# Optimization experiments

Hardware: AMD Instinct MI355X
Metric: run time of the kernel (lower is better)

## Reference

```python
import jax, jax.numpy as jnp
import numpy as np

VOCAB = 32000
DIM = 1024
HID = 4096
MAXLEN = 2048
NH = 2       # number of sequential LowRankLinearAttention layers
KD = 64      # key_dim hardcoded in the module
B = 2
L = 2048


def setup_inputs() -> dict:
    key = jax.random.key(0)
    ks = jax.random.split(key, 12)
    def rn(k, shape, scale):
        return jax.random.normal(k, shape, dtype=jnp.float32) * scale
    return {
        "input_indices": jax.random.randint(ks[0], (B, L), 0, VOCAB),
        "token_embed": rn(ks[1], (VOCAB, DIM), 0.02),
        "pos_embed": rn(ks[2], (MAXLEN, DIM), 0.02),
        # per-layer attention projections (stored [in, out]; x @ W == torch Linear)
        "Wq": rn(ks[3], (NH, DIM, KD), DIM ** -0.5),
        "Wk": rn(ks[4], (NH, DIM, KD), DIM ** -0.5),
        "Wv": rn(ks[5], (NH, DIM, KD), DIM ** -0.5),
        "Wo": rn(ks[6], (NH, KD, DIM), KD ** -0.5),
        "norm_g": jnp.ones((NH, DIM), jnp.float32),
        "norm_b": jnp.zeros((NH, DIM), jnp.float32),
        "out_norm_g": jnp.ones((DIM,), jnp.float32),
        "out_norm_b": jnp.zeros((DIM,), jnp.float32),
        "W1": rn(ks[7], (DIM, HID), DIM ** -0.5),
        "b1": jnp.zeros((HID,), jnp.float32),
        "W2": rn(ks[8], (HID, VOCAB), HID ** -0.5),
        "b2": jnp.zeros((VOCAB,), jnp.float32),
    }


def _layernorm(x, g, b, eps=1e-5):
    m = jnp.mean(x, axis=-1, keepdims=True)
    v = jnp.var(x, axis=-1, keepdims=True)
    return (x - m) / jnp.sqrt(v + eps) * g + b


def _lowrank_linear_attn(x, Wq, Wk, Wv, Wo):
    # x: [B,L,D]; Q,K,V: [B,L,k]
    Q = jax.nn.elu(x @ Wq) + 1.0
    K = jax.nn.elu(x @ Wk) + 1.0
    V = x @ Wv
    # causal prefix sums of outer products K_t V_t^T -> [B,L,k,k]
    KV_sum = jnp.cumsum(K[..., :, None] * V[..., None, :], axis=1)
    K_sum = jnp.cumsum(K, axis=1)
    num = jnp.einsum('blk,blkj->blj', Q, KV_sum)          # [B,L,k]
    den = jnp.einsum('blk,blk->bl', Q, K_sum)[..., None]  # [B,L,1]
    return (num / (den + 1e-6)) @ Wo


def reference(input_indices, token_embed, pos_embed, Wq, Wk, Wv, Wo,
              norm_g, norm_b, out_norm_g, out_norm_b, W1, b1, W2, b2):
    seq_len = input_indices.shape[1]
    x = token_embed[input_indices] + pos_embed[jnp.arange(seq_len)]
    for i in range(Wq.shape[0]):
        x = x + _lowrank_linear_attn(x, Wq[i], Wk[i], Wv[i], Wo[i])
        x = _layernorm(x, norm_g[i], norm_b[i])
    x = _layernorm(x, out_norm_g, out_norm_b)
    h = jax.nn.gelu(x @ W1 + b1, approximate=False)  # torch nn.GELU default = erf
    logits = h @ W2 + b2
    return logits
```

## Files before the change

kernel.cpp:

```cpp
#include <hip/hip_runtime.h>

typedef __attribute__((ext_vector_type(4))) float  f4;
typedef __attribute__((ext_vector_type(2))) float  f2;
typedef __attribute__((ext_vector_type(4))) unsigned short us4;
typedef __attribute__((ext_vector_type(8))) short  s8;
typedef __attribute__((ext_vector_type(4))) float  f32x4;

__device__ __forceinline__ unsigned short f2bf(float f) {
  unsigned u = __float_as_uint(f);
  u += 0x7fffu + ((u >> 16) & 1u);
  return (unsigned short)(u >> 16);
}
__device__ __forceinline__ float elu1(float x) { return x > 0.f ? x + 1.f : __expf(x); }
__device__ __forceinline__ float gelu_erf(float x) { return 0.5f * x * (1.f + erff(x * 0.70710678118654752f)); }

__device__ __forceinline__ void async16(const void* g, void* l) {
  __builtin_amdgcn_global_load_lds((const __attribute__((address_space(1))) void*)g,
                                   (__attribute__((address_space(3))) void*)l, 16, 0, 0);
}

__device__ __forceinline__ void rawbar() {
  asm volatile("s_barrier" ::: "memory");
}

__device__ __forceinline__ unsigned l2u(const void* p) {
  return (unsigned)(size_t)(const __attribute__((address_space(3))) char*)p;
}
template<int OFF>
__device__ __forceinline__ void dsr(s8& d, unsigned base) {
  asm volatile("ds_read_b128 %0, %1 offset:%2" : "=v"(d) : "v"(base), "i"(OFF));
}

__global__ __launch_bounds__(256) void embed_kernel(
    const int* __restrict__ idx, const float* __restrict__ tok,
    const float* __restrict__ pos, float* __restrict__ X, unsigned short* __restrict__ XB)
{
  int g = blockIdx.x * 256 + threadIdx.x;
  int t = g >> 8;
  int c4 = (g & 255) * 4;
  int l = t & 2047;
  int tk = idx[t];
  f4 v = *(const f4*)(tok + (size_t)tk * 1024 + c4);
  f4 p = *(const f4*)(pos + (size_t)l * 1024 + c4);
  v += p;
  *(f4*)(X + (size_t)t * 1024 + c4) = v;
  us4 o = { f2bf(v[0]), f2bf(v[1]), f2bf(v[2]), f2bf(v[3]) };
  *(us4*)(XB + (size_t)t * 1024 + c4) = o;
}

__global__ __launch_bounds__(256) void transpose_cvt(
    const float* __restrict__ src, unsigned short* __restrict__ dst, int N, int K)
{
  __shared__ unsigned short t[64][72];
  int k0 = blockIdx.x * 64, n0 = blockIdx.y * 64;
  int tid = threadIdx.x;
#pragma unroll
  for (int i = 0; i < 4; ++i) {
    int f = tid + i * 256;
    int r = f >> 4, c4 = (f & 15) * 4;
    f4 v = *(const f4*)(src + (size_t)(k0 + r) * N + n0 + c4);
    us4 o = { f2bf(v[0]), f2bf(v[1]), f2bf(v[2]), f2bf(v[3]) };
    *(us4*)&t[r][c4] = o;
  }
  __syncthreads();
#pragma unroll
  for (int i = 0; i < 4; ++i) {
    int f = tid + i * 256;
    int nr = f >> 4, kc4 = (f & 15) * 4;
    us4 o = { t[kc4 + 0][nr], t[kc4 + 1][nr], t[kc4 + 2][nr], t[kc4 + 3][nr] };
    *(us4*)(dst + (size_t)(n0 + nr) * K + k0 + kc4) = o;
  }
}

template<int EPI, int BF32>
__global__ __launch_bounds__(256) void gemm_bt(
    const unsigned short* __restrict__ A, const unsigned short* __restrict__ Bt,
    const float* __restrict__ Bf, const float* __restrict__ bias,
    void* __restrict__ Cv, int M, int N, int K, int mtiles)
{
  __shared__ unsigned short As[128 * 32];
  __shared__ unsigned short Bs[128 * 32];
  int bid = blockIdx.x;
  int mt = bid % mtiles, nt = bid / mtiles;
  int m0 = mt * 128, n0 = nt * 128;
  int tid = threadIdx.x, lane = tid & 63, w = tid >> 6;
  int wm = (w & 1) * 64, wn = (w >> 1) * 64;

  int c0 = w * 128 + lane, c1 = c0 + 64;
  size_t aO0 = (size_t)(m0 + (c0 >> 2)) * K + (size_t)((c0 & 3) * 8);
  size_t aO1 = (size_t)(m0 + (c1 >> 2)) * K + (size_t)((c1 & 3) * 8);
  size_t bO0 = (size_t)(n0 + (c0 >> 2)) * K + (size_t)((c0 & 3) * 8);
  size_t bO1 = (size_t)(n0 + (c1 >> 2)) * K + (size_t)((c1 & 3) * 8);
  unsigned short* lA0 = As + (w * 128) * 8;
  unsigned short* lA1 = As + (w * 128 + 64) * 8;
  unsigned short* lB0 = Bs + (w * 128) * 8;
  unsigned short* lB1 = Bs + (w * 128 + 64) * 8;

  f32x4 acc[4][4];
  f32x4 zz = {0.f, 0.f, 0.f, 0.f};
#pragma unroll
  for (int i = 0; i < 4; ++i)
#pragma unroll
    for (int j = 0; j < 4; ++j) acc[i][j] = zz;

  int rr = lane & 15, kh = (lane >> 4) * 8;
  const unsigned short* Ar = As + (wm + rr) * 32 + kh;
  const unsigned short* Br = Bs + (wn + rr) * 32 + kh;

  for (int k0 = 0; k0 < K; k0 += 32) {
    async16(A + aO0 + k0, lA0);
    async16(A + aO1 + k0, lA1);
    if constexpr (!BF32) {
      async16(Bt + bO0 + k0, lB0);
      async16(Bt + bO1 + k0, lB1);
    } else {
#pragma unroll
      for (int i = 0; i < 4; ++i) {
        int f = tid + i * 256;
        int kr = f >> 5, c4 = (f & 31) * 4;
        f4 v = *(const f4*)(Bf + (size_t)(k0 + kr) * N + n0 + c4);
#pragma unroll
        for (int e = 0; e < 4; ++e) Bs[(c4 + e) * 32 + kr] = f2bf(v[e]);
      }
    }
    __syncthreads();
    s8 af[4], bfr[4];
#pragma unroll
    for (int mi = 0; mi < 4; ++mi) af[mi] = *(const s8*)(Ar + mi * 512);
#pragma unroll
    for (int ni = 0; ni < 4; ++ni) bfr[ni] = *(const s8*)(Br + ni * 512);
#pragma unroll
    for (int mi = 0; mi < 4; ++mi)
#pragma unroll
      for (int ni = 0; ni < 4; ++ni)
        acc[mi][ni] = __builtin_amdgcn_mfma_f32_16x16x32_bf16(af[mi], bfr[ni], acc[mi][ni], 0, 0, 0);
    __syncthreads();
  }

  int cr = (lane >> 4) * 4;
#pragma unroll
  for (int mi = 0; mi < 4; ++mi) {
#pragma unroll
    for (int ni = 0; ni < 4; ++ni) {
      int gc = n0 + wn + ni * 16 + rr;
      float bv = (EPI > 0) ? bias[gc] : 0.f;
#pragma unroll
      for (int r = 0; r < 4; ++r) {
        int gr = m0 + wm + mi * 16 + cr + r;
        float v = acc[mi][ni][r] + bv;
        if constexpr (EPI == 1) {
          ((unsigned short*)Cv)[(size_t)gr * N + gc] = f2bf(gelu_erf(v));
        } else {
          ((float*)Cv)[(size_t)gr * N + gc] = v;
        }
      }
    }
  }
}

template<int EPI>
__global__ __launch_bounds__(512) void gemm2(
    const unsigned short* __restrict__ A, const unsigned short* __restrict__ Bt,
    const float* __restrict__ bias, void* __restrict__ Cv,
    int M, int N, int K, int mtiles)
{
  __shared__ __align__(16) char A0r[32768];
  __shared__ __align__(16) char B0r[32768];
  __shared__ __align__(16) char A1r[32768];
  __shared__ __align__(16) char B1r[32768];

  const int tid = threadIdx.x, lane = tid & 63, w = tid >> 6;
  const int wm = w >> 2, wn = w & 3;
  const int NT = K >> 6;

  int nwg = gridDim.x, orig = blockIdx.x;
  int q = nwg >> 3, r = nwg & 7;
  int xcd = orig & 7, lin = orig >> 3;
  int swz = (xcd < r ? xcd * (q + 1) : r * (q + 1) + (xcd - r) * q) + lin;
  int mt = swz % mtiles, nt = swz / mtiles;
  int m0 = mt * 256, n0 = nt * 256;

  const size_t klane8 = (size_t)((lane >> 4) << 3);
  const size_t arow0 = (size_t)(m0 + w * 32 + (lane & 15)) * K;
  const size_t arow1 = arow0 + (size_t)16 * K;
  const size_t brow0 = (size_t)(n0 + w * 32 + (lane & 15)) * K;
  const size_t brow1 = brow0 + (size_t)16 * K;

  auto stgA = [&](char* reg, int kt, int kb) {
    int ktc = kt < NT ? kt : NT - 1;
    size_t kk = (size_t)ktc * 64 + (size_t)(kb * 32) + klane8;
    char* d = reg + w * 4096 + kb * 1024;
    async16(A + arow0 + kk, d);
    async16(A + arow1 + kk, d + 2048);
  };
  auto stgB = [&](char* reg, int kt, int kb) {
    int ktc = kt < NT ? kt : NT - 1;
    size_t kk = (size_t)ktc * 64 + (size_t)(kb * 32) + klane8;
    char* d = reg + w * 4096 + kb * 1024;
    async16(Bt + brow0 + kk, d);
    async16(Bt + brow1 + kk, d + 2048);
  };

  const unsigned AB0 = l2u(A0r + wm * 16384 + lane * 16);
  const unsigned BB0 = l2u(B0r + wn * 8192 + lane * 16);
  const unsigned AB1 = l2u(A1r + wm * 16384 + lane * 16);
  const unsigned BB1 = l2u(B1r + wn * 8192 + lane * 16);

  f32x4 acc[8][4];
  f32x4 zz = {0.f, 0.f, 0.f, 0.f};
#pragma unroll
  for (int i = 0; i < 8; ++i)
#pragma unroll
    for (int j = 0; j < 4; ++j) acc[i][j] = zz;

  stgA(A0r, 0, 0); stgA(A0r, 0, 1); stgB(B0r, 0, 0); stgB(B0r, 0, 1);
  stgA(A1r, 1, 0); stgA(A1r, 1, 1); stgB(B1r, 1, 0); stgB(B1r, 1, 1);
  asm volatile("s_waitcnt vmcnt(8)" ::: "memory");
  rawbar();

  for (int t = 0; t < NT; ++t) {
    const int odd = t & 1;
    const unsigned AB = odd ? AB1 : AB0;
    const unsigned BB = odd ? BB1 : BB0;
    char* Ad = odd ? A1r : A0r;
    char* Bd = odd ? B1r : B0r;

    s8 bf[8], af[16];
    dsr<(0 * 2 + 0) * 1024>(bf[0], BB);
    dsr<(0 * 2 + 1) * 1024>(bf[1], BB);
    dsr<(1 * 2 + 0) * 1024>(bf[2], BB);
    dsr<(1 * 2 + 1) * 1024>(bf[3], BB);
    dsr<(2 * 2 + 0) * 1024>(bf[4], BB);
    dsr<(2 * 2 + 1) * 1024>(bf[5], BB);
    dsr<(3 * 2 + 0) * 1024>(bf[6], BB);
    dsr<(3 * 2 + 1) * 1024>(bf[7], BB);
    dsr<(0 * 2 + 0) * 1024>(af[0], AB);
    dsr<(0 * 2 + 1) * 1024>(af[1], AB);
    dsr<(1 * 2 + 0) * 1024>(af[2], AB);
    dsr<(1 * 2 + 1) * 1024>(af[3], AB);
    dsr<(2 * 2 + 0) * 1024>(af[4], AB);
    dsr<(2 * 2 + 1) * 1024>(af[5], AB);
    dsr<(3 * 2 + 0) * 1024>(af[6], AB);
    dsr<(3 * 2 + 1) * 1024>(af[7], AB);
    dsr<(4 * 2 + 0) * 1024>(af[8], AB);
    dsr<(4 * 2 + 1) * 1024>(af[9], AB);
    dsr<(5 * 2 + 0) * 1024>(af[10], AB);
    dsr<(5 * 2 + 1) * 1024>(af[11], AB);
    dsr<(6 * 2 + 0) * 1024>(af[12], AB);
    dsr<(6 * 2 + 1) * 1024>(af[13], AB);
    dsr<(7 * 2 + 0) * 1024>(af[14], AB);
    dsr<(7 * 2 + 1) * 1024>(af[15], AB);

    asm volatile("s_waitcnt lgkmcnt(12)" ::: "memory");
    __builtin_amdgcn_sched_barrier(0);
    __builtin_amdgcn_s_setprio(1);
#pragma unroll
    for (int ni = 0; ni < 4; ++ni) {
#pragma unroll
      for (int f = 0; f < 2; ++f) {
        acc[f][ni] = __builtin_amdgcn_mfma_f32_16x16x32_bf16(af[f * 2 + 0], bf[ni * 2 + 0], acc[f][ni], 0, 0, 0);
        acc[f][ni] = __builtin_amdgcn_mfma_f32_16x16x32_bf16(af[f * 2 + 1], bf[ni * 2 + 1], acc[f][ni], 0, 0, 0);
      }
    }
    __builtin_amdgcn_s_setprio(0);
    asm volatile("s_waitcnt lgkmcnt(8)" ::: "memory");
    __builtin_amdgcn_sched_barrier(0);
    __builtin_amdgcn_s_setprio(1);
#pragma unroll
    for (int ni = 0; ni < 4; ++ni) {
#pragma unroll
      for (int f = 2; f < 4; ++f) {
        acc[f][ni] = __builtin_amdgcn_mfma_f32_16x16x32_bf16(af[f * 2 + 0], bf[ni * 2 + 0], acc[f][ni], 0, 0, 0);
        acc[f][ni] = __builtin_amdgcn_mfma_f32_16x16x32_bf16(af[f * 2 + 1], bf[ni * 2 + 1], acc[f][ni], 0, 0, 0);
      }
    }
    __builtin_amdgcn_s_setprio(0);
    asm volatile("s_waitcnt lgkmcnt(4)" ::: "memory");
    __builtin_amdgcn_sched_barrier(0);
    __builtin_amdgcn_s_setprio(1);
#pragma unroll
    for (int ni = 0; ni < 4; ++ni) {
#pragma unroll
      for (int f = 4; f < 6; ++f) {
        acc[f][ni] = __builtin_amdgcn_mfma_f32_16x16x32_bf16(af[f * 2 + 0], bf[ni * 2 + 0], acc[f][ni], 0, 0, 0);
        acc[f][ni] = __builtin_amdgcn_mfma_f32_16x16x32_bf16(af[f * 2 + 1], bf[ni * 2 + 1], acc[f][ni], 0, 0, 0);
      }
    }
    __builtin_amdgcn_s_setprio(0);
    asm volatile("s_waitcnt lgkmcnt(0)" ::: "memory");
    __builtin_amdgcn_sched_barrier(0);
    __builtin_amdgcn_s_setprio(1);
#pragma unroll
    for (int ni = 0; ni < 4; ++ni) {
#pragma unroll
      for (int f = 6; f < 8; ++f) {
        acc[f][ni] = __builtin_amdgcn_mfma_f32_16x16x32_bf16(af[f * 2 + 0], bf[ni * 2 + 0], acc[f][ni], 0, 0, 0);
        acc[f][ni] = __builtin_amdgcn_mfma_f32_16x16x32_bf16(af[f * 2 + 1], bf[ni * 2 + 1], acc[f][ni], 0, 0, 0);
      }
    }
    __builtin_amdgcn_s_setprio(0);
    __builtin_amdgcn_sched_barrier(0);

    stgA(Ad, t + 2, 0); stgA(Ad, t + 2, 1);
    stgB(Bd, t + 2, 0); stgB(Bd, t + 2, 1);
    asm volatile("s_waitcnt vmcnt(8)" ::: "memory");
    rawbar();
  }

  asm volatile("s_waitcnt vmcnt(0) lgkmcnt(0)" ::: "memory");
  __builtin_amdgcn_sched_barrier(0);

  int rr = lane & 15, cr = (lane >> 4) * 4;
#pragma unroll
  for (int f = 0; f < 8; ++f) {
#pragma unroll
    for (int ni = 0; ni < 4; ++ni) {
      int gc = n0 + wn * 64 + ni * 16 + rr;
      float bv = bias[gc];
#pragma unroll
      for (int rg = 0; rg < 4; ++rg) {
        int gr = m0 + wm * 128 + f * 16 + cr + rg;
        float v = acc[f][ni][rg] + bv;
        if constexpr (EPI == 1) {
          ((unsigned short*)Cv)[(size_t)gr * N + gc] = f2bf(gelu_erf(v));
        } else {
          ((float*)Cv)[(size_t)gr * N + gc] = v;
        }
      }
    }
  }
}

__global__ __launch_bounds__(256) void chunk_sums(
    const float* __restrict__ QKV, float* __restrict__ KVc, float* __restrict__ Ksum)
{
  __shared__ float Ks[64][68], Vs[64][68];
  int blk = blockIdx.x, t0 = blk * 64, tid = threadIdx.x;
#pragma unroll
  for (int i = 0; i < 4; ++i) {
    int f = tid + i * 256;
    int r = f >> 4, c4 = (f & 15) * 4;
    const float* s = QKV + (size_t)(t0 + r) * 256;
    f4 k = *(const f4*)(s + 64 + c4);
    f4 v = *(const f4*)(s + 128 + c4);
#pragma unroll
    for (int e = 0; e < 4; ++e) { Ks[r][c4 + e] = elu1(k[e]); Vs[r][c4 + e] = v[e]; }
  }
  __syncthreads();
  int i0 = tid >> 2, jb = (tid & 3) * 16;
  f4 a0 = {0,0,0,0}, a1 = {0,0,0,0}, a2 = {0,0,0,0}, a3 = {0,0,0,0};
  for (int t = 0; t < 64; ++t) {
    float kk = Ks[t][i0];
    a0 += kk * (*(const f4*)&Vs[t][jb]);
    a1 += kk * (*(const f4*)&Vs[t][jb + 4]);
    a2 += kk * (*(const f4*)&Vs[t][jb + 8]);
    a3 += kk * (*(const f4*)&Vs[t][jb + 12]);
  }
  float* d = KVc + (size_t)blk * 4096 + i0 * 64 + jb;
  *(f4*)(d) = a0; *(f4*)(d + 4) = a1; *(f4*)(d + 8) = a2; *(f4*)(d + 12) = a3;
  if (tid < 64) {
    float s = 0.f;
    for (int t = 0; t < 64; ++t) s += Ks[t][tid];
    Ksum[(size_t)blk * 64 + tid] = s;
  }
}

__global__ __launch_bounds__(256) void prefix_state(
    const float* __restrict__ KVc, const float* __restrict__ Ksum,
    float* __restrict__ KVp, float* __restrict__ Ksump)
{
  int b = blockIdx.x >> 3, seg = blockIdx.x & 7;
  int e = seg * 512 + threadIdx.x * 2;
  f2 run = {0.f, 0.f};
#pragma unroll
  for (int c = 0; c < 32; ++c) {
    size_t base = ((size_t)b * 32 + c) * 4096 + e;
    *(f2*)(KVp + base) = run;
    run += *(const f2*)(KVc + base);
  }
  if (seg == 0 && threadIdx.x < 64) {
    float rs = 0.f; int i = threadIdx.x;
#pragma unroll
    for (int c = 0; c < 32; ++c) {
      size_t base = ((size_t)b * 32 + c) * 64 + i;
      Ksump[base] = rs;
      rs += Ksum[base];
    }
  }
}

__global__ __launch_bounds__(256) void attn_ns(
    const float* __restrict__ QKV, const float* __restrict__ KVp,
    const float* __restrict__ Ksump, float* __restrict__ NsG)
{
  __shared__ float Qs[64][68], Ks[64][68], Vs[64][68], Ss[64][68], Ps[64][68];
  __shared__ float ksps[64];
  int blk = blockIdx.x, t0 = blk * 64, tid = threadIdx.x;
#pragma unroll
  for (int i = 0; i < 4; ++i) {
    int f = tid + i * 256;
    int r = f >> 4, c4 = (f & 15) * 4;
    const float* s = QKV + (size_t)(t0 + r) * 256;
    f4 q = *(const f4*)(s + c4);
    f4 k = *(const f4*)(s + 64 + c4);
    f4 v = *(const f4*)(s + 128 + c4);
    f4 p = *(const f4*)(KVp + (size_t)blk * 4096 + r * 64 + c4);
#pragma unroll
    for (int e = 0; e < 4; ++e) {
      Qs[r][c4 + e] = elu1(q[e]); Ks[r][c4 + e] = elu1(k[e]);
      Vs[r][c4 + e] = v[e];       Ps[r][c4 + e] = p[e];
    }
  }
  if (tid < 64) ksps[tid] = Ksump[(size_t)blk * 64 + tid];
  __syncthreads();
  int tq = tid >> 2, jb = (tid & 3) * 16;
#pragma unroll
  for (int jj = 0; jj < 16; ++jj) {
    int tk = jb + jj;
    float s = 0.f;
    if (tk <= tq) {
#pragma unroll
      for (int k4 = 0; k4 < 16; ++k4) {
        f4 q = *(const f4*)&Qs[tq][k4 * 4];
        f4 k = *(const f4*)&Ks[tk][k4 * 4];
        s += q[0] * k[0] + q[1] * k[1] + q[2] * k[2] + q[3] * k[3];
      }
    }
    Ss[tq][tk] = s;
  }
  __syncthreads();
  f4 a0 = {0,0,0,0}, a1 = {0,0,0,0}, a2 = {0,0,0,0}, a3 = {0,0,0,0};
  for (int t = 0; t < 64; ++t) {
    float s = Ss[tq][t];
    a0 += s * (*(const f4*)&Vs[t][jb]);
    a1 += s * (*(const f4*)&Vs[t][jb + 4]);
    a2 += s * (*(const f4*)&Vs[t][jb + 8]);
    a3 += s * (*(const f4*)&Vs[t][jb + 12]);
  }
  for (int k = 0; k < 64; ++k) {
    float q = Qs[tq][k];
    a0 += q * (*(const f4*)&Ps[k][jb]);
    a1 += q * (*(const f4*)&Ps[k][jb + 4]);
    a2 += q * (*(const f4*)&Ps[k][jb + 8]);
    a3 += q * (*(const f4*)&Ps[k][jb + 12]);
  }
  float den = 0.f;
  for (int t = 0; t < 64; ++t) den += Ss[tq][t];
  for (int k = 0; k < 64; ++k) den += Qs[tq][k] * ksps[k];
  float inv = 1.f / (den + 1e-6f);
  float* d = NsG + (size_t)(t0 + tq) * 64 + jb;
  *(f4*)(d)      = a0 * inv;
  *(f4*)(d + 4)  = a1 * inv;
  *(f4*)(d + 8)  = a2 * inv;
  *(f4*)(d + 12) = a3 * inv;
}

__global__ __launch_bounds__(256) void attn_apply(
    const float* __restrict__ NsG, const float* __restrict__ Wo, float* __restrict__ X)
{
  __shared__ float Ns[64][68];
  __shared__ float Wt[64][260];
  int chunk = blockIdx.x >> 2, dg = blockIdx.x & 3;
  int t0 = chunk * 64, d0 = dg * 256, tid = threadIdx.x;
#pragma unroll
  for (int i = 0; i < 4; ++i) {
    int f = tid + i * 256;
    int r = f >> 4, c4 = (f & 15) * 4;
    *(f4*)&Ns[r][c4] = *(const f4*)(NsG + (size_t)(t0 + r) * 64 + c4);
  }
#pragma unroll
  for (int i = 0; i < 16; ++i) {
    int f = tid + i * 256;
    int r = f >> 6, c4 = (f & 63) * 4;
    *(f4*)&Wt[r][c4] = *(const f4*)(Wo + (size_t)r * 1024 + d0 + c4);
  }
  __syncthreads();
  int w = tid >> 6, lane = tid & 63;
  for (int ts = 0; ts < 16; ++ts) {
    int t = w * 16 + ts;
    float a0 = 0.f, a1 = 0.f, a2 = 0.f, a3 = 0.f;
#pragma unroll
    for (int j = 0; j < 64; ++j) {
      float nv = Ns[t][j];
      a0 += nv * Wt[j][lane];
      a1 += nv * Wt[j][64 + lane];
      a2 += nv * Wt[j][128 + lane];
      a3 += nv * Wt[j][192 + lane];
    }
    size_t o = (size_t)(t0 + t) * 1024 + d0 + lane;
    X[o]       += a0;
    X[o + 64]  += a1;
    X[o + 128] += a2;
    X[o + 192] += a3;
  }
}

__global__ __launch_bounds__(256) void layernorm_kernel(
    float* __restrict__ X, unsigned short* __restrict__ XB,
    const float* __restrict__ g, const float* __restrict__ b)
{
  int t = blockIdx.x * 4 + (threadIdx.x >> 6);
  int lane = threadIdx.x & 63;
  float* row = X + (size_t)t * 1024;
  f4 v[4];
  float s = 0.f, s2 = 0.f;
#pragma unroll
  for (int i = 0; i < 4; ++i) {
    v[i] = *(const f4*)(row + (i * 64 + lane) * 4);
#pragma unroll
    for (int e = 0; e < 4; ++e) { s += v[i][e]; s2 += v[i][e] * v[i][e]; }
  }
#pragma unroll
  for (int off = 32; off > 0; off >>= 1) {
    s  += __shfl_xor(s, off, 64);
    s2 += __shfl_xor(s2, off, 64);
  }
  float mean = s * (1.f / 1024.f);
  float var = s2 * (1.f / 1024.f) - mean * mean;
  float rstd = rsqrtf(var + 1e-5f);
#pragma unroll
  for (int i = 0; i < 4; ++i) {
    int d = (i * 64 + lane) * 4;
    f4 gv = *(const f4*)(g + d);
    f4 bv = *(const f4*)(b + d);
    f4 y;
#pragma unroll
    for (int e = 0; e < 4; ++e) y[e] = (v[i][e] - mean) * rstd * gv[e] + bv[e];
    *(f4*)(row + d) = y;
    us4 o = { f2bf(y[0]), f2bf(y[1]), f2bf(y[2]), f2bf(y[3]) };
    *(us4*)(XB + (size_t)t * 1024 + d) = o;
  }
}

extern "C" void kernel_launch(void* const* d_in, const int* in_sizes, int n_in,
                              void* d_out, int out_size, void* d_ws, size_t ws_size,
                              hipStream_t stream) {
  (void)in_sizes; (void)n_in; (void)out_size;
  const int*   idx = (const int*)d_in[0];
  const float* tok = (const float*)d_in[1];
  const float* pos = (const float*)d_in[2];
  const float* Wq  = (const float*)d_in[3];
  const float* Wk  = (const float*)d_in[4];
  const float* Wv  = (const float*)d_in[5];
  const float* Wo  = (const float*)d_in[6];
  const float* ng  = (const float*)d_in[7];
  const float* nb  = (const float*)d_in[8];
  const float* ong = (const float*)d_in[9];
  const float* onb = (const float*)d_in[10];
  const float* W1  = (const float*)d_in[11];
  const float* b1  = (const float*)d_in[12];
  const float* W2  = (const float*)d_in[13];
  const float* b2  = (const float*)d_in[14];
  float* out = (float*)d_out;
  char* ws = (char*)d_ws;

  float* X            = (float*)(ws + 0);
  unsigned short* XB  = (unsigned short*)(ws + 16777216);
  unsigned short* QT0 = (unsigned short*)(ws + 25165824);
  unsigned short* QT1 = (unsigned short*)(ws + 25690112);
  float* QKVB         = (float*)(ws + 26214400);
  float* KVC          = (float*)(ws + 30408704);
  float* KSUM         = (float*)(ws + 31457280);
  float* KVP          = (float*)(ws + 31490048);
  float* KSP          = (float*)(ws + 32538624);
  unsigned short* W1T = (unsigned short*)(ws + 32571392);
  unsigned short* H   = (unsigned short*)(ws + 40960000);
  unsigned short* W2T = (unsigned short*)(ws + 74514432);
  float* NSG = KVC;
  bool bigws = ws_size >= 336658432ull;

  hipMemsetAsync(QT0, 0, 524288, stream);
  hipMemsetAsync(QT1, 0, 524288, stream);
  transpose_cvt<<<dim3(16, 1), 256, 0, stream>>>(Wq,          QT0,              64, 1024);
  transpose_cvt<<<dim3(16, 1), 256, 0, stream>>>(Wk,          QT0 + 64 * 1024,  64, 1024);
  transpose_cvt<<<dim3(16, 1), 256, 0, stream>>>(Wv,          QT0 + 128 * 1024, 64, 1024);
  transpose_cvt<<<dim3(16, 1), 256, 0, stream>>>(Wq + 65536,  QT1,              64, 1024);
  transpose_cvt<<<dim3(16, 1), 256, 0, stream>>>(Wk + 65536,  QT1 + 64 * 1024,  64, 1024);
  transpose_cvt<<<dim3(16, 1), 256, 0, stream>>>(Wv + 65536,  QT1 + 128 * 1024, 64, 1024);
  transpose_cvt<<<dim3(16, 64), 256, 0, stream>>>(W1, W1T, 4096, 1024);
  if (bigws)
    transpose_cvt<<<dim3(64, 500), 256, 0, stream>>>(W2, W2T, 32000, 4096);

  embed_kernel<<<4096, 256, 0, stream>>>(idx, tok, pos, X, XB);

  for (int layer = 0; layer < 2; ++layer) {
    const unsigned short* QT = layer ? QT1 : QT0;
    gemm_bt<0, 0><<<64, 256, 0, stream>>>(XB, QT, nullptr, nullptr, QKVB, 4096, 256, 1024, 32);
    chunk_sums<<<64, 256, 0, stream>>>(QKVB, KVC, KSUM);
    prefix_state<<<16, 256, 0, stream>>>(KVC, KSUM, KVP, KSP);
    attn_ns<<<64, 256, 0, stream>>>(QKVB, KVP, KSP, NSG);
    attn_apply<<<256, 256, 0, stream>>>(NSG, Wo + (size_t)layer * 65536, X);
    layernorm_kernel<<<1024, 256, 0, stream>>>(X, XB, ng + layer * 1024, nb + layer * 1024);
  }
  layernorm_kernel<<<1024, 256, 0, stream>>>(X, XB, ong, onb);

  gemm_bt<1, 0><<<1024, 256, 0, stream>>>(XB, W1T, nullptr, b1, H, 4096, 4096, 1024, 32);
  if (bigws)
    gemm2<2><<<2000, 512, 0, stream>>>(H, W2T, b2, out, 4096, 32000, 4096, 16);
  else
    gemm_bt<2, 1><<<8000, 256, 0, stream>>>(H, nullptr, W2, b2, out, 4096, 32000, 4096, 32);
}
```

Baseline: 1.599 ms.

## Software-pipeline LDS fragment reads across k-halves in big GEMM, reuse for FFN1

Restructures the 256x256 GEMM main loop so LDS fragment reads for the next k-half or the next tile are issued while MFMAs on the current fragments run. The final quarter of MFMAs for a tile is deferred past the barrier so it overlaps the next tile's fragment reads. It also splits the fragment registers into two halves, which lowers peak register use. The W1 GEMM now uses this large-tile kernel (256 blocks of 512 threads) in place of the smaller gemm_bt, which risks low occupancy since 256 blocks may underfill the CUs.

```diff
diff --git a/kernel.cpp b/kernel.cpp
--- a/kernel.cpp
+++ b/kernel.cpp
@@ -159,7 +159,7 @@
 }
 
 template<int EPI>
-__global__ __launch_bounds__(512) void gemm2(
+__global__ __launch_bounds__(512) void gemm3(
     const unsigned short* __restrict__ A, const unsigned short* __restrict__ Bt,
     const float* __restrict__ bias, void* __restrict__ Cv,
     int M, int N, int K, int mtiles)
@@ -212,99 +212,113 @@
   for (int i = 0; i < 8; ++i)
 #pragma unroll
     for (int j = 0; j < 4; ++j) acc[i][j] = zz;
+  s8 af0[8], af1[8], bf0[4], bf1[4];
+
+  auto readC0 = [&](unsigned AB, unsigned BB) {
+    dsr<(0 * 2 + 0) * 1024>(af0[0], AB);
+    dsr<(1 * 2 + 0) * 1024>(af0[1], AB);
+    dsr<(2 * 2 + 0) * 1024>(af0[2], AB);
+    dsr<(3 * 2 + 0) * 1024>(af0[3], AB);
+    dsr<(4 * 2 + 0) * 1024>(af0[4], AB);
+    dsr<(5 * 2 + 0) * 1024>(af0[5], AB);
+    dsr<(6 * 2 + 0) * 1024>(af0[6], AB);
+    dsr<(7 * 2 + 0) * 1024>(af0[7], AB);
+    dsr<(0 * 2 + 0) * 1024>(bf0[0], BB);
+    dsr<(1 * 2 + 0) * 1024>(bf0[1], BB);
+  };
+  auto readC1 = [&](unsigned BB) {
+    dsr<(2 * 2 + 0) * 1024>(bf0[2], BB);
+    dsr<(3 * 2 + 0) * 1024>(bf0[3], BB);
+  };
+  auto readC2 = [&](unsigned AB, unsigned BB) {
+    dsr<(0 * 2 + 1) * 1024>(af1[0], AB);
+    dsr<(1 * 2 + 1) * 1024>(af1[1], AB);
+    dsr<(2 * 2 + 1) * 1024>(af1[2], AB);
+    dsr<(3 * 2 + 1) * 1024>(af1[3], AB);
+    dsr<(4 * 2 + 1) * 1024>(af1[4], AB);
+    dsr<(5 * 2 + 1) * 1024>(af1[5], AB);
+    dsr<(6 * 2 + 1) * 1024>(af1[6], AB);
+    dsr<(7 * 2 + 1) * 1024>(af1[7], AB);
+    dsr<(0 * 2 + 1) * 1024>(bf1[0], BB);
+    dsr<(1 * 2 + 1) * 1024>(bf1[1], BB);
+  };
+  auto readC3 = [&](unsigned BB) {
+    dsr<(2 * 2 + 1) * 1024>(bf1[2], BB);
+    dsr<(3 * 2 + 1) * 1024>(bf1[3], BB);
+  };
 
   stgA(A0r, 0, 0); stgA(A0r, 0, 1); stgB(B0r, 0, 0); stgB(B0r, 0, 1);
   stgA(A1r, 1, 0); stgA(A1r, 1, 1); stgB(B1r, 1, 0); stgB(B1r, 1, 1);
   asm volatile("s_waitcnt vmcnt(8)" ::: "memory");
   rawbar();
+  readC0(AB0, BB0);
+  readC1(BB0);
 
   for (int t = 0; t < NT; ++t) {
     const int odd = t & 1;
     const unsigned AB = odd ? AB1 : AB0;
     const unsigned BB = odd ? BB1 : BB0;
+    const unsigned ABn = odd ? AB0 : AB1;
+    const unsigned BBn = odd ? BB0 : BB1;
     char* Ad = odd ? A1r : A0r;
     char* Bd = odd ? B1r : B0r;
 
-    s8 bf[8], af[16];
-    dsr<(0 * 2 + 0) * 1024>(bf[0], BB);
-    dsr<(0 * 2 + 1) * 1024>(bf[1], BB);
-    dsr<(1 * 2 + 0) * 1024>(bf[2], BB);
-    dsr<(1 * 2 + 1) * 1024>(bf[3], BB);
-    dsr<(2 * 2 + 0) * 1024>(bf[4], BB);
-    dsr<(2 * 2 + 1) * 1024>(bf[5], BB);
-    dsr<(3 * 2 + 0) * 1024>(bf[6], BB);
-    dsr<(3 * 2 + 1) * 1024>(bf[7], BB);
-    dsr<(0 * 2 + 0) * 1024>(af[0], AB);
-    dsr<(0 * 2 + 1) * 1024>(af[1], AB);
-    dsr<(1 * 2 + 0) * 1024>(af[2], AB);
-    dsr<(1 * 2 + 1) * 1024>(af[3], AB);
-    dsr<(2 * 2 + 0) * 1024>(af[4], AB);
-    dsr<(2 * 2 + 1) * 1024>(af[5], AB);
-    dsr<(3 * 2 + 0) * 1024>(af[6], AB);
-    dsr<(3 * 2 + 1) * 1024>(af[7], AB);
-    dsr<(4 * 2 + 0) * 1024>(af[8], AB);
-    dsr<(4 * 2 + 1) * 1024>(af[9], AB);
-    dsr<(5 * 2 + 0) * 1024>(af[10], AB);
-    dsr<(5 * 2 + 1) * 1024>(af[11], AB);
-    dsr<(6 * 2 + 0) * 1024>(af[12], AB);
-    dsr<(6 * 2 + 1) * 1024>(af[13], AB);
-    dsr<(7 * 2 + 0) * 1024>(af[14], AB);
-    dsr<(7 * 2 + 1) * 1024>(af[15], AB);
-
-    asm volatile("s_waitcnt lgkmcnt(12)" ::: "memory");
+    asm volatile("s_waitcnt lgkmcnt(2)" ::: "memory");
     __builtin_amdgcn_sched_barrier(0);
     __builtin_amdgcn_s_setprio(1);
 #pragma unroll
-    for (int ni = 0; ni < 4; ++ni) {
-#pragma unroll
-      for (int f = 0; f < 2; ++f) {
-        acc[f][ni] = __builtin_amdgcn_mfma_f32_16x16x32_bf16(af[f * 2 + 0], bf[ni * 2 + 0], acc[f][ni], 0, 0, 0);
-        acc[f][ni] = __builtin_amdgcn_mfma_f32_16x16x32_bf16(af[f * 2 + 1], bf[ni * 2 + 1], acc[f][ni], 0, 0, 0);
-      }
+    for (int f = 0; f < 8; ++f) {
+      acc[f][0] = __builtin_amdgcn_mfma_f32_16x16x32_bf16(af0[f], bf0[0], acc[f][0], 0, 0, 0);
+      acc[f][1] = __builtin_amdgcn_mfma_f32_16x16x32_bf16(af0[f], bf0[1], acc[f][1], 0, 0, 0);
     }
     __builtin_amdgcn_s_setprio(0);
-    asm volatile("s_waitcnt lgkmcnt(8)" ::: "memory");
+    __builtin_amdgcn_sched_barrier(0);
+
+    readC2(AB, BB);
+
+    asm volatile("s_waitcnt lgkmcnt(10)" ::: "memory");
     __builtin_amdgcn_sched_barrier(0);
     __builtin_amdgcn_s_setprio(1);
 #pragma unroll
-    for (int ni = 0; ni < 4; ++ni) {
-#pragma unroll
-      for (int f = 2; f < 4; ++f) {
-        acc[f][ni] = __builtin_amdgcn_mfma_f32_16x16x32_bf16(af[f * 2 + 0], bf[ni * 2 + 0], acc[f][ni], 0, 0, 0);
-        acc[f][ni] = __builtin_amdgcn_mfma_f32_16x16x32_bf16(af[f * 2 + 1], bf[ni * 2 + 1], acc[f][ni], 0, 0, 0);
-      }
+    for (int f = 0; f < 8; ++f) {
+      acc[f][2] = __builtin_amdgcn_mfma_f32_16x16x32_bf16(af0[f], bf0[2], acc[f][2], 0, 0, 0);
+      acc[f][3] = __builtin_amdgcn_mfma_f32_16x16x32_bf16(af0[f], bf0[3], acc[f][3], 0, 0, 0);
     }
     __builtin_amdgcn_s_setprio(0);
-    asm volatile("s_waitcnt lgkmcnt(4)" ::: "memory");
+    __builtin_amdgcn_sched_barrier(0);
+
+    readC3(BB);
+
+    asm volatile("s_waitcnt lgkmcnt(2)" ::: "memory");
     __builtin_amdgcn_sched_barrier(0);
     __builtin_amdgcn_s_setprio(1);
 #pragma unroll
-    for (int ni = 0; ni < 4; ++ni) {
-#pragma unroll
-      for (int f = 4; f < 6; ++f) {
-        acc[f][ni] = __builtin_amdgcn_mfma_f32_16x16x32_bf16(af[f * 2 + 0], bf[ni * 2 + 0], acc[f][ni], 0, 0, 0);
-        acc[f][ni] = __builtin_amdgcn_mfma_f32_16x16x32_bf16(af[f * 2 + 1], bf[ni * 2 + 1], acc[f][ni], 0, 0, 0);
-      }
+    for (int f = 0; f < 8; ++f) {
+      acc[f][0] = __builtin_amdgcn_mfma_f32_16x16x32_bf16(af1[f], bf1[0], acc[f][0], 0, 0, 0);
+      acc[f][1] = __builtin_amdgcn_mfma_f32_16x16x32_bf16(af1[f], bf1[1], acc[f][1], 0, 0, 0);
     }
     __builtin_amdgcn_s_setprio(0);
+    __builtin_amdgcn_sched_barrier(0);
+
     asm volatile("s_waitcnt lgkmcnt(0)" ::: "memory");
     __builtin_amdgcn_sched_barrier(0);
-    __builtin_amdgcn_s_setprio(1);
-#pragma unroll
-    for (int ni = 0; ni < 4; ++ni) {
-#pragma unroll
-      for (int f = 6; f < 8; ++f) {
-        acc[f][ni] = __builtin_amdgcn_mfma_f32_16x16x32_bf16(af[f * 2 + 0], bf[ni * 2 + 0], acc[f][ni], 0, 0, 0);
-        acc[f][ni] = __builtin_amdgcn_mfma_f32_16x16x32_bf16(af[f * 2 + 1], bf[ni * 2 + 1], acc[f][ni], 0, 0, 0);
-      }
-    }
-    __builtin_amdgcn_s_setprio(0);
-    __builtin_amdgcn_sched_barrier(0);
-
     stgA(Ad, t + 2, 0); stgA(Ad, t + 2, 1);
     stgB(Bd, t + 2, 0); stgB(Bd, t + 2, 1);
+
     asm volatile("s_waitcnt vmcnt(8)" ::: "memory");
     rawbar();
+
+    readC0(ABn, BBn);
+    readC1(BBn);
+
+    __builtin_amdgcn_s_setprio(1);
+#pragma unroll
+    for (int f = 0; f < 8; ++f) {
+      acc[f][2] = __builtin_amdgcn_mfma_f32_16x16x32_bf16(af1[f], bf1[2], acc[f][2], 0, 0, 0);
+      acc[f][3] = __builtin_amdgcn_mfma_f32_16x16x32_bf16(af1[f], bf1[3], acc[f][3], 0, 0, 0);
+    }
+    __builtin_amdgcn_s_setprio(0);
+    __builtin_amdgcn_sched_barrier(0);
   }
 
   asm volatile("s_waitcnt vmcnt(0) lgkmcnt(0)" ::: "memory");
@@ -594,9 +608,9 @@
   }
   layernorm_kernel<<<1024, 256, 0, stream>>>(X, XB, ong, onb);
 
-  gemm_bt<1, 0><<<1024, 256, 0, stream>>>(XB, W1T, nullptr, b1, H, 4096, 4096, 1024, 32);
+  gemm3<1><<<256, 512, 0, stream>>>(XB, W1T, b1, H, 4096, 4096, 1024, 16);
   if (bigws)
-    gemm2<2><<<2000, 512, 0, stream>>>(H, W2T, b2, out, 4096, 32000, 4096, 16);
+    gemm3<2><<<2000, 512, 0, stream>>>(H, W2T, b2, out, 4096, 32000, 4096, 16);
   else
     gemm_bt<2, 1><<<8000, 256, 0, stream>>>(H, nullptr, W2, b2, out, 4096, 32000, 4096, 32);
 }
```

Result: no change. 1.602 ms (+0.2%).
